# Kernel tuning notes

Hardware: AMD Instinct MI355X
Metric: run time of the kernel (lower is better)

## Reference

```python
import jax, jax.numpy as jnp
import numpy as np

KS = 3          # kernel_size
M = 6           # num_bases
TEM = 6         # tem_size = (KS//2)*num_bases
BN_EPS = 1e-3   # keras BatchNormalization default epsilon


def _conv(x, w):
    # x: NCHW, w: OIHW, stride 1, SAME padding (module uses padding='same')
    return jax.lax.conv_general_dilated(x, w, (1, 1), 'SAME',
                                        dimension_numbers=('NCHW', 'OIHW', 'NCHW'))


def _bn(x, gamma, beta, mean, var):
    # inference-mode batchnorm over channel dim (NCHW)
    s = gamma * jax.lax.rsqrt(var + BN_EPS)
    return x * s[None, :, None, None] + (beta - mean * s)[None, :, None, None]


def _unfold(x):
    # im2col: N,C,H,W -> N,C,KS*KS,H,W with SAME padding, stride 1
    N, C, H, W = x.shape
    xp = jnp.pad(x, ((0, 0), (0, 0), (1, 1), (1, 1)))
    taps = [xp[:, :, i:i + H, j:j + W] for i in range(KS) for j in range(KS)]
    return jnp.stack(taps, axis=2)


def setup_inputs() -> dict:
    key = jax.random.key(0)
    ks = jax.random.split(key, 16)
    N, C, O, H, W = 16, 128, 128, 64, 64
    inter, bsz = 64, M * TEM  # 64, 36
    x = jax.random.normal(ks[0], (N, C, H, W), jnp.float32)
    w1 = jax.random.normal(ks[1], (inter, C, 3, 3), jnp.float32) * (1.0 / np.sqrt(C * 9))
    gamma1 = jnp.ones((inter,), jnp.float32)
    beta1 = jnp.zeros((inter,), jnp.float32)
    mean1 = jax.random.normal(ks[2], (inter,), jnp.float32) * 0.1
    var1 = jax.random.uniform(ks[3], (inter,), jnp.float32, 0.5, 1.5)
    w2 = jax.random.normal(ks[4], (bsz, inter, 3, 3), jnp.float32) * (1.0 / np.sqrt(inter * 9))
    gamma2 = jnp.ones((bsz,), jnp.float32)
    beta2 = jnp.zeros((bsz,), jnp.float32)
    mean2 = jax.random.normal(ks[5], (bsz,), jnp.float32) * 0.1
    var2 = jax.random.uniform(ks[6], (bsz,), jnp.float32, 0.5, 1.5)
    # Fixed Fourier-Bessel-style basis [TEM, KS*KS], normalized as in calculate_FB_bases
    rng = np.random.RandomState(0)
    psi = rng.normal(size=(KS * KS, TEM)).astype(np.float32)
    c = np.sqrt((psi ** 2).sum(0).mean())
    fb_bases = jnp.asarray((psi / c).T)  # [TEM, 9]
    coef = jax.random.normal(ks[7], (O, C * M), jnp.float32) * np.sqrt(2.0 / (C * M))
    bias = jnp.zeros((O,), jnp.float32)
    return {'x': x, 'w1': w1, 'gamma1': gamma1, 'beta1': beta1, 'mean1': mean1,
            'var1': var1, 'w2': w2, 'gamma2': gamma2, 'beta2': beta2,
            'mean2': mean2, 'var2': var2, 'fb_bases': fb_bases, 'coef': coef,
            'bias': bias}


def reference(x, w1, gamma1, beta1, mean1, var1, w2, gamma2, beta2, mean2, var2,
              fb_bases, coef, bias):
    N, C, H, W = x.shape
    # bases_net: conv3x3 -> BN -> tanh -> conv3x3 -> BN -> tanh
    h = jnp.tanh(_bn(_conv(x, w1), gamma1, beta1, mean1, var1))
    b = jnp.tanh(_bn(_conv(h, w2), gamma2, beta2, mean2, var2))   # N,36,H,W
    bcoef = b.reshape(N, M, TEM, H, W)
    # combine predicted coefficients with fixed FB bases -> per-pixel filters
    bases = jnp.einsum('bmkhw,kl->bmlhw', bcoef, fb_bases)        # N,M,9,H,W
    xu = _unfold(x)                                               # N,C,9,H,W
    # per-pixel gather-multiply-reduce over the 9 taps
    bo = jnp.einsum('bmlhw,bclhw->bcmhw', bases, xu)              # N,C,M,H,W
    bo = bo.reshape(N, C * M, H, W)
    # 1x1 conv with coef + bias
    out = jnp.einsum('bkhw,ok->bohw', bo, coef) + bias[None, :, None, None]
    return out
```

## Files before the change

kernel.cpp:

```cpp
#include <hip/hip_runtime.h>
#include <hip/hip_bf16.h>

using bf16 = __hip_bfloat16;
typedef __attribute__((ext_vector_type(8))) short bf16x8;
typedef __attribute__((ext_vector_type(4))) float f32x4;

#define BN_EPS 1e-3f

#define OFF_FLAG  0u
#define OFF_W1M   16u
#define OFF_B1F   36880u
#define OFF_W2M   36944u
#define OFF_B2F   50768u
#define OFF_FBF   50804u
#define OFF_CFM   50860u
#define OFF_BIASF 100012u
#define OFF_BB    100144u

__device__ __forceinline__ float b2f(bf16 v) { return __bfloat162float(v); }
__device__ __forceinline__ unsigned short f2b(float f) {
    union { bf16 h; unsigned short u; } cv;
    cv.h = __float2bfloat16(f);
    return cv.u;
}
__device__ __forceinline__ unsigned packbf(float a, float b) {
    return (unsigned)f2b(a) | ((unsigned)f2b(b) << 16);
}
__device__ __forceinline__ float ldin(const void* p, long long i, int f) {
    return f ? b2f(((const bf16*)p)[i]) : ((const float*)p)[i];
}
__device__ __forceinline__ float lo_f(unsigned u) { return __uint_as_float(u << 16); }
__device__ __forceinline__ float hi_f(unsigned u) { return __uint_as_float(u & 0xFFFF0000u); }
__device__ __forceinline__ void ld8f(const void* p, long long i, int f, float* o) {
    if (f) {
        uint4 v = *(const uint4*)((const unsigned short*)p + i);
        o[0] = lo_f(v.x); o[1] = hi_f(v.x); o[2] = lo_f(v.y); o[3] = hi_f(v.y);
        o[4] = lo_f(v.z); o[5] = hi_f(v.z); o[6] = lo_f(v.w); o[7] = hi_f(v.w);
    } else {
        const float* q = (const float*)p + i;
        float4 a = *(const float4*)q, b = *(const float4*)(q + 4);
        o[0] = a.x; o[1] = a.y; o[2] = a.z; o[3] = a.w;
        o[4] = b.x; o[5] = b.y; o[6] = b.z; o[7] = b.w;
    }
}
__device__ __forceinline__ bf16x8 lds_frag(const unsigned short* p) {
    uint2 lo = *(const uint2*)p;
    uint2 hi = *(const uint2*)(p + 4);
    union { unsigned u[4]; bf16x8 v; } r;
    r.u[0] = lo.x; r.u[1] = lo.y; r.u[2] = hi.x; r.u[3] = hi.y;
    return r.v;
}

__global__ void detect_kernel(const void* __restrict__ g1, float* __restrict__ ws) {
    if (threadIdx.x == 0) {
        unsigned w = ((const unsigned*)g1)[0];
        ws[OFF_FLAG] = (w == 0x3F800000u) ? 0.f : 1.f;
    }
}

__global__ __launch_bounds__(256) void prep_kernel(
    const void* __restrict__ w1, const void* __restrict__ g1, const void* __restrict__ be1,
    const void* __restrict__ mu1, const void* __restrict__ va1,
    const void* __restrict__ w2, const void* __restrict__ g2, const void* __restrict__ be2,
    const void* __restrict__ mu2, const void* __restrict__ va2,
    const void* __restrict__ fb, const void* __restrict__ coef, const void* __restrict__ bias,
    float* __restrict__ ws)
{
    const int f = (ws[OFF_FLAG] != 0.f);
    int j = blockIdx.x * 256 + threadIdx.x;
    if (j < 73728) {
        int tap = j >> 13, r = j & 8191;
        int ntile = r >> 11, r2 = r & 2047;
        int ks = r2 >> 9, r3 = r2 & 511;
        int lane = r3 >> 3, jj = r3 & 7;
        int oc = ntile * 16 + (lane & 15);
        int ic = ks * 32 + (lane >> 4) * 8 + jj;
        float s = ldin(g1, oc, f) * rsqrtf(ldin(va1, oc, f) + BN_EPS);
        ((unsigned short*)(ws + OFF_W1M))[j] = f2b(ldin(w1, (oc * 128 + ic) * 9 + tap, f) * s);
        return;
    }
    j -= 73728;
    if (j < 64) {
        float s = ldin(g1, j, f) * rsqrtf(ldin(va1, j, f) + BN_EPS);
        ws[OFF_B1F + j] = ldin(be1, j, f) - ldin(mu1, j, f) * s;
        return;
    }
    j -= 64;
    if (j < 27648) {
        int tap = j / 3072, r = j - tap * 3072;
        int ntile = r >> 10, r2 = r & 1023;
        int ks = r2 >> 9, r3 = r2 & 511;
        int lane = r3 >> 3, jj = r3 & 7;
        int oc = ntile * 16 + (lane & 15);
        int ic = ks * 32 + (lane >> 4) * 8 + jj;
        float v = 0.f;
        if (oc < 36) {
            float s = ldin(g2, oc, f) * rsqrtf(ldin(va2, oc, f) + BN_EPS);
            v = ldin(w2, (oc * 64 + ic) * 9 + tap, f) * s;
        }
        ((unsigned short*)(ws + OFF_W2M))[j] = f2b(v);
        return;
    }
    j -= 27648;
    if (j < 36) {
        float s = ldin(g2, j, f) * rsqrtf(ldin(va2, j, f) + BN_EPS);
        ws[OFF_B2F + j] = ldin(be2, j, f) - ldin(mu2, j, f) * s;
        return;
    }
    j -= 36;
    if (j < 54) { ws[OFF_FBF + j] = ldin(fb, j, f); return; }
    j -= 54;
    if (j < 98304) {
        int chunk = j / 12288, r = j - chunk * 12288;
        int ks = r >> 12, r2 = r & 4095;
        int ntile = r2 >> 9, r3 = r2 & 511;
        int lane = r3 >> 3, jj = r3 & 7;
        int o = ntile * 16 + (lane & 15);
        int k = chunk * 96 + ks * 32 + (lane >> 4) * 8 + jj;
        ((unsigned short*)(ws + OFF_CFM))[j] = f2b(ldin(coef, o * 768 + k, f));
        return;
    }
    j -= 98304;
    if (j < 128) { ws[OFF_BIASF + j] = ldin(bias, j, f); return; }
}

__global__ __launch_bounds__(256) void conv1_mfma(
    const void* __restrict__ x, const float* __restrict__ ws,
    unsigned short* __restrict__ hbuf)
{
    __shared__ unsigned short sA[3][66][132];
    unsigned* sAu = (unsigned*)sA;
    const unsigned short* w1m = (const unsigned short*)(ws + OFF_W1M);
    const int f = (ws[OFF_FLAG] != 0.f);
    const int t = threadIdx.x;
    const int n = blockIdx.x >> 6, h = blockIdx.x & 63;

    for (int e = t; e < 396; e += 256) {
        int dy = e / 132, q = e - dy * 132;
        int wrow = (q >= 66) ? 65 : 0;
        int cu = (q >= 66) ? q - 66 : q;
        sAu[(dy * 66 + wrow) * 66 + cu] = 0u;
    }
    {
        const long long xb = (long long)n * 128 * 4096;
        for (int u = t; u < 1536; u += 256) {
            int dy = u >> 9, rem = u & 511, icp = rem >> 3, w8 = rem & 7;
            int hh = h + dy - 1;
            float va[8], vb[8];
            if (hh >= 0 && hh < 64) {
                long long base = xb + (long long)(icp * 2) * 4096 + hh * 64 + w8 * 8;
                ld8f(x, base, f, va);
                ld8f(x, base + 4096, f, vb);
            } else {
#pragma unroll
                for (int i = 0; i < 8; ++i) { va[i] = 0.f; vb[i] = 0.f; }
            }
            const int wb_ = w8 * 8 + 1;
#pragma unroll
            for (int i = 0; i < 8; ++i)
                sAu[(dy * 66 + wb_ + i) * 66 + icp] = packbf(va[i], vb[i]);
        }
    }
    __syncthreads();

    const int wv = t >> 6, lane = t & 63;
    const int fr = lane & 15, quad = lane >> 4;
    const int mh = (wv & 1) * 32, nh = (wv >> 1) * 32;
    const int ntb = nh >> 4;

    f32x4 acc[2][2];
#pragma unroll
    for (int i = 0; i < 2; ++i)
#pragma unroll
        for (int j = 0; j < 2; ++j) acc[i][j] = (f32x4){0.f, 0.f, 0.f, 0.f};

#pragma unroll
    for (int tap = 0; tap < 9; ++tap) {
        const int dy = tap / 3, dx = tap - dy * 3;
#pragma unroll
        for (int ks = 0; ks < 4; ++ks) {
            const int kof = ks * 32 + quad * 8;
            bf16x8 a0 = lds_frag(&sA[dy][mh + fr + dx][kof]);
            bf16x8 a1 = lds_frag(&sA[dy][mh + 16 + fr + dx][kof]);
            bf16x8 b0 = *(const bf16x8*)(w1m + (((tap * 4 + ntb) * 4 + ks) * 64 + lane) * 8);
            bf16x8 b1 = *(const bf16x8*)(w1m + (((tap * 4 + ntb + 1) * 4 + ks) * 64 + lane) * 8);
            acc[0][0] = __builtin_amdgcn_mfma_f32_16x16x32_bf16(a0, b0, acc[0][0], 0, 0, 0);
            acc[0][1] = __builtin_amdgcn_mfma_f32_16x16x32_bf16(a0, b1, acc[0][1], 0, 0, 0);
            acc[1][0] = __builtin_amdgcn_mfma_f32_16x16x32_bf16(a1, b0, acc[1][0], 0, 0, 0);
            acc[1][1] = __builtin_amdgcn_mfma_f32_16x16x32_bf16(a1, b1, acc[1][1], 0, 0, 0);
        }
    }

#pragma unroll
    for (int mt = 0; mt < 2; ++mt)
#pragma unroll
        for (int nt = 0; nt < 2; ++nt) {
            int oc = nh + nt * 16 + fr;
            int m0 = mh + mt * 16 + quad * 4;
            float bv = ws[OFF_B1F + oc];
            f32x4 v = acc[mt][nt];
            union { unsigned short us[4]; uint2 u; } pk;
#pragma unroll
            for (int i = 0; i < 4; ++i) pk.us[i] = f2b(tanhf(v[i] + bv));
            *(uint2*)(hbuf + (size_t)(n * 64 + oc) * 4096 + h * 64 + m0) = pk.u;
        }
}

__global__ __launch_bounds__(256) void conv2_mfma(
    const float* __restrict__ ws, const unsigned short* __restrict__ hbuf,
    float* __restrict__ bbout)
{
    __shared__ unsigned short sA[3][66][68];
    unsigned* sAu = (unsigned*)sA;
    const unsigned short* w2m = (const unsigned short*)(ws + OFF_W2M);
    const int t = threadIdx.x;
    const int n = blockIdx.x >> 6, h = blockIdx.x & 63;

    for (int e = t; e < 204; e += 256) {
        int dy = e / 68, q = e - dy * 68;
        int wrow = (q >= 34) ? 65 : 0;
        int cu = (q >= 34) ? q - 34 : q;
        sAu[(dy * 66 + wrow) * 34 + cu] = 0u;
    }
    {
        const unsigned short* hn = hbuf + (size_t)n * 64 * 4096;
        for (int u = t; u < 768; u += 256) {
            int dy = u >> 8, rem = u & 255, icp = rem >> 3, w8 = rem & 7;
            int hh = h + dy - 1;
            uint4 a = make_uint4(0u, 0u, 0u, 0u), b = a;
            if (hh >= 0 && hh < 64) {
                const unsigned short* p = hn + (size_t)(icp * 2) * 4096 + hh * 64 + w8 * 8;
                a = *(const uint4*)p;
                b = *(const uint4*)(p + 4096);
            }
            const int wb_ = w8 * 8 + 1;
            unsigned au[4] = {a.x, a.y, a.z, a.w}, bu[4] = {b.x, b.y, b.z, b.w};
#pragma unroll
            for (int jj = 0; jj < 4; ++jj) {
                unsigned lo = (au[jj] & 0xFFFFu) | (bu[jj] << 16);
                unsigned hi = (au[jj] >> 16) | (bu[jj] & 0xFFFF0000u);
                sAu[(dy * 66 + wb_ + 2 * jj) * 34 + icp] = lo;
                sAu[(dy * 66 + wb_ + 2 * jj + 1) * 34 + icp] = hi;
            }
        }
    }
    __syncthreads();

    const int wv = t >> 6, lane = t & 63;
    const int fr = lane & 15, quad = lane >> 4;
    const int m0 = wv * 16;

    f32x4 acc[3];
#pragma unroll
    for (int i = 0; i < 3; ++i) acc[i] = (f32x4){0.f, 0.f, 0.f, 0.f};

#pragma unroll
    for (int tap = 0; tap < 9; ++tap) {
        const int dy = tap / 3, dx = tap - dy * 3;
#pragma unroll
        for (int ks = 0; ks < 2; ++ks) {
            const int kof = ks * 32 + quad * 8;
            bf16x8 a = lds_frag(&sA[dy][m0 + fr + dx][kof]);
#pragma unroll
            for (int nt = 0; nt < 3; ++nt) {
                bf16x8 b = *(const bf16x8*)(w2m + (((tap * 3 + nt) * 2 + ks) * 64 + lane) * 8);
                acc[nt] = __builtin_amdgcn_mfma_f32_16x16x32_bf16(a, b, acc[nt], 0, 0, 0);
            }
        }
    }

    const int pbase = (n << 12) + h * 64 + m0 + quad * 4;
#pragma unroll
    for (int nt = 0; nt < 3; ++nt) {
        int oc = nt * 16 + fr;
        if (oc < 36) {
            float bv = ws[OFF_B2F + oc];
            f32x4 v = acc[nt];
#pragma unroll
            for (int reg = 0; reg < 4; ++reg)
                bbout[(size_t)(pbase + reg) * 36 + oc] = tanhf(v[reg] + bv);
        }
    }
}

__global__ __launch_bounds__(512) void fuse_kernel(
    const void* __restrict__ x, const float* __restrict__ ws, void* __restrict__ outv)
{
    __shared__ float sbaseT[54][64];
    __shared__ __align__(16) unsigned short slbo[64][104];
    __shared__ __align__(16) unsigned short sX[3][66][20];
    unsigned* sXu = (unsigned*)sX;

    const float* bbp = ws + OFF_BB;
    const float* fbf = ws + OFF_FBF;
    const unsigned short* cfm = (const unsigned short*)(ws + OFF_CFM);
    const int f = (ws[OFF_FLAG] != 0.f);

    const int t = threadIdx.x;
    const int p0 = blockIdx.x * 64;
    const int n = p0 >> 12;
    const int h = (p0 >> 6) & 63;

    for (int task = t; task < 64 * 54; task += 512) {
        int p = task & 63, j = task >> 6;
        int m = j / 9, l = j - m * 9;
        const float* br = bbp + (size_t)(p0 + p) * 36 + m * 6;
        float s = 0.f;
#pragma unroll
        for (int k = 0; k < 6; ++k) s += br[k] * fbf[k * 9 + l];
        sbaseT[j][p] = s;
    }
    if (t < 48) {
        int dy = t >> 4, q = t & 15;
        int wrow = (q >= 8) ? 65 : 0;
        sXu[(dy * 66 + wrow) * 10 + (q & 7)] = 0u;
    }
    __syncthreads();

    const int pp = t >> 3, cl = t & 7;
    const int wv = t >> 6, lane = t & 63;
    const int fr = lane & 15, quad = lane >> 4;
    const int m0w = (wv & 3) * 16;
    const int nh = (wv >> 2) * 64;
    const int ntb = nh >> 4;

    f32x4 acc[4];
#pragma unroll
    for (int nt = 0; nt < 4; ++nt) acc[nt] = (f32x4){0.f, 0.f, 0.f, 0.f};

    const long long xbase = (long long)n * 128 * 4096;
    const int sw = t & 63, sg = t >> 6;

    for (int c0 = 0; c0 < 128; c0 += 16) {
        const int chunk = c0 >> 4;
#pragma unroll
        for (int u = sg; u < 24; u += 8) {
            int dy = u >> 3, icp = u & 7;
            int hh = h + dy - 1;
            float v0 = 0.f, v1 = 0.f;
            if (hh >= 0 && hh < 64) {
                long long base = xbase + (long long)(c0 + icp * 2) * 4096 + hh * 64 + sw;
                v0 = ldin(x, base, f);
                v1 = ldin(x, base + 4096, f);
            }
            sXu[(dy * 66 + sw + 1) * 10 + icp] = packbf(v0, v1);
        }
        __syncthreads();
        {
            float sm[2][6];
#pragma unroll
            for (int q = 0; q < 2; ++q)
#pragma unroll
                for (int m = 0; m < 6; ++m) sm[q][m] = 0.f;
#pragma unroll
            for (int dy = 0; dy < 3; ++dy)
#pragma unroll
                for (int dx = 0; dx < 3; ++dx) {
                    const int l = dy * 3 + dx;
                    unsigned d = sXu[(dy * 66 + pp + dx) * 10 + cl];
                    float x0 = lo_f(d), x1 = hi_f(d);
#pragma unroll
                    for (int m = 0; m < 6; ++m) {
                        float bv = sbaseT[m * 9 + l][pp];
                        sm[0][m] += bv * x0;
                        sm[1][m] += bv * x1;
                    }
                }
            unsigned* du = (unsigned*)slbo + pp * 52 + cl * 6;
            uint2 w0 = make_uint2(packbf(sm[0][0], sm[0][1]), packbf(sm[0][2], sm[0][3]));
            uint2 w1 = make_uint2(packbf(sm[0][4], sm[0][5]), packbf(sm[1][0], sm[1][1]));
            uint2 w2 = make_uint2(packbf(sm[1][2], sm[1][3]), packbf(sm[1][4], sm[1][5]));
            *(uint2*)&du[0] = w0;
            *(uint2*)&du[2] = w1;
            *(uint2*)&du[4] = w2;
        }
        __syncthreads();
#pragma unroll
        for (int ks = 0; ks < 3; ++ks) {
            const int kof = ks * 32 + quad * 8;
            bf16x8 a = *(const bf16x8*)&slbo[m0w + fr][kof];
            const unsigned short* cb = cfm + ((chunk * 3 + ks) * 8 + ntb) * 512 + lane * 8;
            bf16x8 b0 = *(const bf16x8*)(cb);
            bf16x8 b1 = *(const bf16x8*)(cb + 512);
            bf16x8 b2 = *(const bf16x8*)(cb + 1024);
            bf16x8 b3 = *(const bf16x8*)(cb + 1536);
            acc[0] = __builtin_amdgcn_mfma_f32_16x16x32_bf16(a, b0, acc[0], 0, 0, 0);
            acc[1] = __builtin_amdgcn_mfma_f32_16x16x32_bf16(a, b1, acc[1], 0, 0, 0);
            acc[2] = __builtin_amdgcn_mfma_f32_16x16x32_bf16(a, b2, acc[2], 0, 0, 0);
            acc[3] = __builtin_amdgcn_mfma_f32_16x16x32_bf16(a, b3, acc[3], 0, 0, 0);
        }
    }

    const int mrow = m0w + quad * 4;
#pragma unroll
    for (int nt = 0; nt < 4; ++nt) {
        int o = nh + nt * 16 + fr;
        float bv = ws[OFF_BIASF + o];
        f32x4 v = acc[nt];
        size_t ofs = (size_t)(n * 128 + o) * 4096 + h * 64 + mrow;
        if (f) {
            union { unsigned short us[4]; uint2 u; } pk;
#pragma unroll
            for (int i = 0; i < 4; ++i) pk.us[i] = f2b(v[i] + bv);
            *(uint2*)((unsigned short*)outv + ofs) = pk.u;
        } else {
            float4 w4 = make_float4(v[0] + bv, v[1] + bv, v[2] + bv, v[3] + bv);
            *(float4*)((float*)outv + ofs) = w4;
        }
    }
}

extern "C" void kernel_launch(void* const* d_in, const int* in_sizes, int n_in,
                              void* d_out, int out_size, void* d_ws, size_t ws_size,
                              hipStream_t stream)
{
    float* ws = (float*)d_ws;
    unsigned short* hbuf = (unsigned short*)d_out;

    hipLaunchKernelGGL(detect_kernel, dim3(1), dim3(64), 0, stream, d_in[2], ws);
    hipLaunchKernelGGL(prep_kernel, dim3(782), dim3(256), 0, stream,
                       d_in[1], d_in[2], d_in[3], d_in[4], d_in[5],
                       d_in[6], d_in[7], d_in[8], d_in[9], d_in[10],
                       d_in[11], d_in[12], d_in[13], ws);
    hipLaunchKernelGGL(conv1_mfma, dim3(1024), dim3(256), 0, stream, d_in[0], ws, hbuf);
    hipLaunchKernelGGL(conv2_mfma, dim3(1024), dim3(256), 0, stream, ws, hbuf, ws + OFF_BB);
    hipLaunchKernelGGL(fuse_kernel, dim3(1024), dim3(512), 0, stream, d_in[0], ws, d_out);
}
```

Measured before the change: 220.5 us.

## Double-buffer input and lbo tiles in fuse kernel, hoist bases into registers

Splits the shared input tile and the per-pixel basis-output tile into two buffers, so the next channel chunk is loaded while the current one is being processed. This cuts each chunk from two barriers to one. Each thread also loads its 54 per-pixel basis values into registers once, instead of re-reading them from LDS on every chunk. The cost is more LDS per block and more registers, which could lower occupancy. The remaining single barrier must still cover both the write-after-read and read-after-write hazards between the buffers.

```diff
diff --git a/kernel.cpp b/kernel.cpp
--- a/kernel.cpp
+++ b/kernel.cpp
@@ -287,8 +287,8 @@
     const void* __restrict__ x, const float* __restrict__ ws, void* __restrict__ outv)
 {
     __shared__ float sbaseT[54][64];
-    __shared__ __align__(16) unsigned short slbo[64][104];
-    __shared__ __align__(16) unsigned short sX[3][66][20];
+    __shared__ __align__(16) unsigned short slbo[2][64][104];
+    __shared__ __align__(16) unsigned short sX[2][3][66][20];
     unsigned* sXu = (unsigned*)sX;
 
     const float* bbp = ws + OFF_BB;
@@ -310,12 +310,13 @@
         for (int k = 0; k < 6; ++k) s += br[k] * fbf[k * 9 + l];
         sbaseT[j][p] = s;
     }
-    if (t < 48) {
-        int dy = t >> 4, q = t & 15;
+    if (t < 96) {
+        int buf = (t >= 48);
+        int e = t - buf * 48;
+        int dy = e >> 4, q = e & 15;
         int wrow = (q >= 8) ? 65 : 0;
-        sXu[(dy * 66 + wrow) * 10 + (q & 7)] = 0u;
-    }
-    __syncthreads();
+        sXu[((buf * 3 + dy) * 66 + wrow) * 10 + (q & 7)] = 0u;
+    }
 
     const int pp = t >> 3, cl = t & 7;
     const int wv = t >> 6, lane = t & 63;
@@ -324,28 +325,49 @@
     const int nh = (wv >> 2) * 64;
     const int ntb = nh >> 4;
 
-    f32x4 acc[4];
-#pragma unroll
-    for (int nt = 0; nt < 4; ++nt) acc[nt] = (f32x4){0.f, 0.f, 0.f, 0.f};
-
     const long long xbase = (long long)n * 128 * 4096;
     const int sw = t & 63, sg = t >> 6;
 
-    for (int c0 = 0; c0 < 128; c0 += 16) {
-        const int chunk = c0 >> 4;
-#pragma unroll
-        for (int u = sg; u < 24; u += 8) {
-            int dy = u >> 3, icp = u & 7;
-            int hh = h + dy - 1;
-            float v0 = 0.f, v1 = 0.f;
-            if (hh >= 0 && hh < 64) {
-                long long base = xbase + (long long)(c0 + icp * 2) * 4096 + hh * 64 + sw;
-                v0 = ldin(x, base, f);
-                v1 = ldin(x, base + 4096, f);
+#pragma unroll
+    for (int u = sg; u < 24; u += 8) {
+        int dy = u >> 3, icp = u & 7;
+        int hh = h + dy - 1;
+        float v0 = 0.f, v1 = 0.f;
+        if (hh >= 0 && hh < 64) {
+            long long base = xbase + (long long)(icp * 2) * 4096 + hh * 64 + sw;
+            v0 = ldin(x, base, f);
+            v1 = ldin(x, base + 4096, f);
+        }
+        sXu[((0 * 3 + dy) * 66 + sw + 1) * 10 + icp] = packbf(v0, v1);
+    }
+    __syncthreads();
+
+    float sb[54];
+#pragma unroll
+    for (int j = 0; j < 54; ++j) sb[j] = sbaseT[j][pp];
+
+    f32x4 acc[4];
+#pragma unroll
+    for (int nt = 0; nt < 4; ++nt) acc[nt] = (f32x4){0.f, 0.f, 0.f, 0.f};
+
+#pragma unroll
+    for (int chunk = 0; chunk < 8; ++chunk) {
+        const int cur = chunk & 1;
+        if (chunk < 7) {
+            const int c0n = (chunk + 1) * 16;
+#pragma unroll
+            for (int u = sg; u < 24; u += 8) {
+                int dy = u >> 3, icp = u & 7;
+                int hh = h + dy - 1;
+                float v0 = 0.f, v1 = 0.f;
+                if (hh >= 0 && hh < 64) {
+                    long long base = xbase + (long long)(c0n + icp * 2) * 4096 + hh * 64 + sw;
+                    v0 = ldin(x, base, f);
+                    v1 = ldin(x, base + 4096, f);
+                }
+                sXu[(((cur ^ 1) * 3 + dy) * 66 + sw + 1) * 10 + icp] = packbf(v0, v1);
             }
-            sXu[(dy * 66 + sw + 1) * 10 + icp] = packbf(v0, v1);
-        }
-        __syncthreads();
+        }
         {
             float sm[2][6];
 #pragma unroll
@@ -357,16 +379,16 @@
 #pragma unroll
                 for (int dx = 0; dx < 3; ++dx) {
                     const int l = dy * 3 + dx;
-                    unsigned d = sXu[(dy * 66 + pp + dx) * 10 + cl];
+                    unsigned d = sXu[((cur * 3 + dy) * 66 + pp + dx) * 10 + cl];
                     float x0 = lo_f(d), x1 = hi_f(d);
 #pragma unroll
                     for (int m = 0; m < 6; ++m) {
-                        float bv = sbaseT[m * 9 + l][pp];
+                        float bv = sb[m * 9 + l];
                         sm[0][m] += bv * x0;
                         sm[1][m] += bv * x1;
                     }
                 }
-            unsigned* du = (unsigned*)slbo + pp * 52 + cl * 6;
+            unsigned* du = (unsigned*)slbo[cur] + pp * 52 + cl * 6;
             uint2 w0 = make_uint2(packbf(sm[0][0], sm[0][1]), packbf(sm[0][2], sm[0][3]));
             uint2 w1 = make_uint2(packbf(sm[0][4], sm[0][5]), packbf(sm[1][0], sm[1][1]));
             uint2 w2 = make_uint2(packbf(sm[1][2], sm[1][3]), packbf(sm[1][4], sm[1][5]));
@@ -378,7 +400,7 @@
 #pragma unroll
         for (int ks = 0; ks < 3; ++ks) {
             const int kof = ks * 32 + quad * 8;
-            bf16x8 a = *(const bf16x8*)&slbo[m0w + fr][kof];
+            bf16x8 a = *(const bf16x8*)&slbo[cur][m0w + fr][kof];
             const unsigned short* cb = cfm + ((chunk * 3 + ks) * 8 + ntb) * 512 + lane * 8;
             bf16x8 b0 = *(const bf16x8*)(cb);
             bf16x8 b1 = *(const bf16x8*)(cb + 512);
```

Result: slower. 249.6 us (+13.2%).
